# Performance work log

Hardware: AMD Instinct MI355X
Metric: run time of the kernel (lower is better)

The kernel has to match this reference:

```python
import jax, jax.numpy as jnp
import numpy as np

HIDDEN = 512
ATT_DIM = 128
LN_EPS = 1e-3  # keras LayerNormalization default epsilon


def setup_inputs() -> dict:
    key = jax.random.key(0)
    k1, k2, k3, k4 = jax.random.split(key, 4)
    hidden_states = jax.random.normal(k1, (64, 2048, HIDDEN), dtype=jnp.float32)
    # Glorot-uniform style init for the dense weights
    def glorot(k, shape):
        lim = np.sqrt(6.0 / (shape[0] + shape[1]))
        return jax.random.uniform(k, shape, jnp.float32, -lim, lim)
    W_a = glorot(k2, (HIDDEN, ATT_DIM))
    U_a = glorot(k3, (HIDDEN, ATT_DIM))
    v_a = glorot(k4, (ATT_DIM, 1))
    ln_gamma = jnp.ones((HIDDEN,), jnp.float32)
    ln_beta = jnp.zeros((HIDDEN,), jnp.float32)
    return {"hidden_states": hidden_states, "W_a": W_a, "U_a": U_a,
            "v_a": v_a, "ln_gamma": ln_gamma, "ln_beta": ln_beta}


def reference(hidden_states, W_a, U_a, v_a, ln_gamma, ln_beta):
    # hidden_states: (B, L, H)
    h_att = jnp.einsum('blh,ha->bla', hidden_states, W_a)        # (B, L, A)
    context = jnp.mean(hidden_states, axis=1, keepdims=True)     # (B, 1, H)
    u_att = jnp.einsum('blh,ha->bla', context, U_a)              # (B, 1, A) broadcasts
    combined = jnp.tanh(h_att + u_att)                           # (B, L, A)
    scores = jnp.einsum('bla,ao->bl', combined, v_a)             # (B, L)
    attn = jax.nn.softmax(scores, axis=-1)                       # (B, L)
    attended = jnp.einsum('blh,bl->bh', hidden_states, attn)     # (B, H)
    # LayerNormalization over last axis
    mu = jnp.mean(attended, axis=-1, keepdims=True)
    var = jnp.var(attended, axis=-1, keepdims=True)
    normed = (attended - mu) * jax.lax.rsqrt(var + LN_EPS)
    out = normed * ln_gamma + ln_beta
    return out, attn
```

## Files before the change

### kernel.cpp

```cpp
#include <hip/hip_runtime.h>
#include <hip/hip_bf16.h>

#define HIDDEN 512
#define ATT    128
#define NB     64
#define SL     2048
#define LN_EPS 1e-3f

typedef __attribute__((ext_vector_type(8))) short short8;
typedef __attribute__((ext_vector_type(4))) float f32x4;

__device__ __forceinline__ short f2bf(float f) {
    union { float f; unsigned u; } v; v.f = f;
    unsigned r = v.u + 0x7fffu + ((v.u >> 16) & 1u);
    return (short)(r >> 16);
}
__device__ __forceinline__ unsigned pack2bf(float lo, float hi) {
    union { __hip_bfloat162 h; unsigned u; } v;
    v.h = __float22bfloat162_rn(make_float2(lo, hi));
    return v.u;
}
__device__ __forceinline__ float bflo(unsigned u) {
    union { unsigned x; float f; } v; v.x = u << 16; return v.f;
}
__device__ __forceinline__ float bfhi(unsigned u) {
    union { unsigned x; float f; } v; v.x = u & 0xffff0000u; return v.f;
}
__device__ __forceinline__ float tanh_fast(float x) {
    float cx = fminf(fmaxf(x, -15.f), 15.f);
    float e = __expf(2.f * cx);
    return (e - 1.f) * __builtin_amdgcn_rcpf(e + 1.f);
}

__global__ void p0_wt(const float* __restrict__ W, short* __restrict__ Wt) {
    int idx = blockIdx.x * 256 + threadIdx.x;
    int a = idx >> 9, h = idx & 511;
    Wt[idx] = f2bf(W[h * ATT + a]);
}

__launch_bounds__(256, 3)
__global__ void p1_gemm_ctx(const float* __restrict__ hidden, const short* __restrict__ Wt,
                            short* __restrict__ h_att, float* __restrict__ ctx_part) {
    int t = threadIdx.x;
    int wave = t >> 6, lane = t & 63, quad = lane >> 4, cb = lane & 15;
    int row0 = blockIdx.x * 128;

    f32x4 acc[2][8];
    #pragma unroll
    for (int mt = 0; mt < 2; ++mt)
        #pragma unroll
        for (int nt = 0; nt < 8; ++nt)
            acc[mt][nt] = (f32x4){0.f, 0.f, 0.f, 0.f};

    const float* aptr0 = hidden + (size_t)(row0 + wave * 32 + cb) * HIDDEN + quad * 8;
    const float* aptr1 = aptr0 + (size_t)16 * HIDDEN;
    const short* bptr  = Wt + (size_t)cb * HIDDEN + quad * 8;
    float* cptr = ctx_part + (size_t)(blockIdx.x * 4 + wave) * HIDDEN + quad * 8;

    #pragma unroll 2
    for (int k0 = 0; k0 < HIDDEN; k0 += 32) {
        const float4 a0lo = *(const float4*)(aptr0 + k0);
        const float4 a0hi = *(const float4*)(aptr0 + k0 + 4);
        const float4 a1lo = *(const float4*)(aptr1 + k0);
        const float4 a1hi = *(const float4*)(aptr1 + k0 + 4);

        short8 b8[8];
        #pragma unroll
        for (int nt = 0; nt < 8; ++nt)
            b8[nt] = *(const short8*)(bptr + nt * 16 * HIDDEN + k0);

        float s[8] = { a0lo.x + a1lo.x, a0lo.y + a1lo.y, a0lo.z + a1lo.z, a0lo.w + a1lo.w,
                       a0hi.x + a1hi.x, a0hi.y + a1hi.y, a0hi.z + a1hi.z, a0hi.w + a1hi.w };
        #pragma unroll
        for (int j = 0; j < 8; ++j) {
            s[j] += __shfl_xor(s[j], 1);
            s[j] += __shfl_xor(s[j], 2);
            s[j] += __shfl_xor(s[j], 4);
            s[j] += __shfl_xor(s[j], 8);
        }
        if (cb == 0) {
            #pragma unroll
            for (int j = 0; j < 8; ++j) cptr[k0 + j] = s[j];
        }

        union { short8 s8; unsigned u[4]; } a0p, a1p;
        a0p.u[0] = pack2bf(a0lo.x, a0lo.y); a0p.u[1] = pack2bf(a0lo.z, a0lo.w);
        a0p.u[2] = pack2bf(a0hi.x, a0hi.y); a0p.u[3] = pack2bf(a0hi.z, a0hi.w);
        a1p.u[0] = pack2bf(a1lo.x, a1lo.y); a1p.u[1] = pack2bf(a1lo.z, a1lo.w);
        a1p.u[2] = pack2bf(a1hi.x, a1hi.y); a1p.u[3] = pack2bf(a1hi.z, a1hi.w);

        #pragma unroll
        for (int nt = 0; nt < 8; ++nt) {
            acc[0][nt] = __builtin_amdgcn_mfma_f32_16x16x32_bf16(a0p.s8, b8[nt], acc[0][nt], 0, 0, 0);
            acc[1][nt] = __builtin_amdgcn_mfma_f32_16x16x32_bf16(a1p.s8, b8[nt], acc[1][nt], 0, 0, 0);
        }
    }

    uint2* hp = (uint2*)h_att;
    size_t base = (((size_t)blockIdx.x * 4 + wave) * 2) * 8 * 64 + lane;
    #pragma unroll
    for (int mt = 0; mt < 2; ++mt)
        #pragma unroll
        for (int nt = 0; nt < 8; ++nt) {
            uint2 p;
            p.x = pack2bf(acc[mt][nt][0], acc[mt][nt][1]);
            p.y = pack2bf(acc[mt][nt][2], acc[mt][nt][3]);
            hp[base + ((size_t)mt * 8 + nt) * 64] = p;
        }
}

__launch_bounds__(256)
__global__ void p2_uatt(const float* __restrict__ ctx_part, const float* __restrict__ U,
                        float* __restrict__ uatt) {
    int b = blockIdx.x, t = threadIdx.x;
    __shared__ float cs[HIDDEN];
    __shared__ float ds[256];
    float s0 = 0.f, s1 = 0.f;
    #pragma unroll 4
    for (int c = 0; c < 64; ++c) {
        const float* base = ctx_part + (size_t)(b * 64 + c) * HIDDEN;
        s0 += base[t];
        s1 += base[t + 256];
    }
    cs[t] = s0; cs[t + 256] = s1;
    __syncthreads();
    int a = t & 127, h0 = (t >> 7) * 256;
    float d = 0.f;
    #pragma unroll 8
    for (int h = 0; h < 256; ++h) d += cs[h0 + h] * U[(size_t)(h0 + h) * ATT + a];
    ds[t] = d;
    __syncthreads();
    if (t < 128) uatt[b * ATT + t] = (ds[t] + ds[t + 128]) * (1.f / SL);
}

__launch_bounds__(256)
__global__ void p3_scores(const short* __restrict__ h_att, const float* __restrict__ v_a,
                          const float* __restrict__ uatt, float* __restrict__ scores) {
    int t = threadIdx.x, bx = blockIdx.x;
    int wave = t >> 6, lane = t & 63, quad = lane >> 4, cb = lane & 15;
    int b = bx >> 4;
    int row0 = bx * 128;

    float uv[8], vv[8];
    #pragma unroll
    for (int nt = 0; nt < 8; ++nt) {
        uv[nt] = uatt[b * ATT + nt * 16 + cb];
        vv[nt] = v_a[nt * 16 + cb];
    }

    const uint2* hp = (const uint2*)h_att;
    size_t base = (((size_t)bx * 4 + wave) * 2) * 8 * 64 + lane;

    #pragma unroll
    for (int mt = 0; mt < 2; ++mt) {
        uint2 f[8];
        #pragma unroll
        for (int nt = 0; nt < 8; ++nt) f[nt] = hp[base + ((size_t)mt * 8 + nt) * 64];
        float r[4] = {0.f, 0.f, 0.f, 0.f};
        #pragma unroll
        for (int nt = 0; nt < 8; ++nt) {
            r[0] += vv[nt] * tanh_fast(bflo(f[nt].x) + uv[nt]);
            r[1] += vv[nt] * tanh_fast(bfhi(f[nt].x) + uv[nt]);
            r[2] += vv[nt] * tanh_fast(bflo(f[nt].y) + uv[nt]);
            r[3] += vv[nt] * tanh_fast(bfhi(f[nt].y) + uv[nt]);
        }
        #pragma unroll
        for (int j = 0; j < 4; ++j) {
            r[j] += __shfl_xor(r[j], 1);
            r[j] += __shfl_xor(r[j], 2);
            r[j] += __shfl_xor(r[j], 4);
            r[j] += __shfl_xor(r[j], 8);
        }
        if (cb == 0) {
            #pragma unroll
            for (int j = 0; j < 4; ++j)
                scores[row0 + wave * 32 + mt * 16 + quad * 4 + j] = r[j];
        }
    }
}

__launch_bounds__(256)
__global__ void p4_softmax(float* __restrict__ attn) {
    int b = blockIdx.x, t = threadIdx.x;
    float* p = attn + b * SL;
    __shared__ float red[256];
    float v[8];
    float m = -1e30f;
    #pragma unroll
    for (int i = 0; i < 8; ++i) { v[i] = p[t + i * 256]; m = fmaxf(m, v[i]); }
    red[t] = m; __syncthreads();
    for (int s = 128; s > 0; s >>= 1) { if (t < s) red[t] = fmaxf(red[t], red[t + s]); __syncthreads(); }
    m = red[0]; __syncthreads();
    float sum = 0.f;
    #pragma unroll
    for (int i = 0; i < 8; ++i) { v[i] = __expf(v[i] - m); sum += v[i]; }
    red[t] = sum; __syncthreads();
    for (int s = 128; s > 0; s >>= 1) { if (t < s) red[t] += red[t + s]; __syncthreads(); }
    float inv = 1.f / red[0];
    #pragma unroll
    for (int i = 0; i < 8; ++i) p[t + i * 256] = v[i] * inv;
}

__launch_bounds__(256)
__global__ void p5_attended(const float* __restrict__ hidden, const float* __restrict__ attn,
                            float* __restrict__ att_part) {
    int b = blockIdx.y, c = blockIdx.x, t = threadIdx.x;
    __shared__ float w_s[128];
    __shared__ float4 red_s[128];
    if (t < 128) w_s[t] = attn[b * SL + c * 128 + t];
    __syncthreads();
    int cg = t & 127, half = t >> 7;
    const float* hp = hidden + ((size_t)b * SL + c * 128 + half * 64) * HIDDEN + cg * 4;
    float4 a = {0.f, 0.f, 0.f, 0.f};
    #pragma unroll 4
    for (int l = 0; l < 64; ++l) {
        float w = w_s[half * 64 + l];
        const float4 g = *(const float4*)(hp + (size_t)l * HIDDEN);
        a.x += w * g.x; a.y += w * g.y; a.z += w * g.z; a.w += w * g.w;
    }
    if (half) red_s[cg] = a;
    __syncthreads();
    if (!half) {
        float4 r = red_s[cg];
        a.x += r.x; a.y += r.y; a.z += r.z; a.w += r.w;
        *(float4*)(att_part + ((size_t)(c * NB + b)) * HIDDEN + cg * 4) = a;
    }
}

__launch_bounds__(256)
__global__ void p6_ln(const float* __restrict__ att_part, const float* __restrict__ gamma,
                      const float* __restrict__ beta, float* __restrict__ out) {
    int b = blockIdx.x, t = threadIdx.x;
    float x0 = 0.f, x1 = 0.f;
    #pragma unroll
    for (int c = 0; c < 16; ++c) {
        size_t base = (size_t)(c * NB + b) * HIDDEN;
        x0 += att_part[base + t];
        x1 += att_part[base + t + 256];
    }
    __shared__ float rs[256], rq[256];
    rs[t] = x0 + x1; rq[t] = x0 * x0 + x1 * x1;
    __syncthreads();
    for (int s = 128; s > 0; s >>= 1) {
        if (t < s) { rs[t] += rs[t + s]; rq[t] += rq[t + s]; }
        __syncthreads();
    }
    float mean = rs[0] * (1.f / HIDDEN);
    float var = rq[0] * (1.f / HIDDEN) - mean * mean;
    float r = rsqrtf(var + LN_EPS);
    out[b * HIDDEN + t]       = (x0 - mean) * r * gamma[t] + beta[t];
    out[b * HIDDEN + t + 256] = (x1 - mean) * r * gamma[t + 256] + beta[t + 256];
}

extern "C" void kernel_launch(void* const* d_in, const int* in_sizes, int n_in,
                              void* d_out, int out_size, void* d_ws, size_t ws_size,
                              hipStream_t stream) {
    const float* hidden = (const float*)d_in[0];
    const float* W      = (const float*)d_in[1];
    const float* U      = (const float*)d_in[2];
    const float* v_a    = (const float*)d_in[3];
    const float* gamma  = (const float*)d_in[4];
    const float* beta   = (const float*)d_in[5];

    float* out  = (float*)d_out;
    float* attn = out + NB * HIDDEN;

    short* h_att    = (short*)d_ws;
    float* ctx_part = (float*)((char*)d_ws + (size_t)NB * SL * ATT * 2);
    float* att_part = ctx_part + (size_t)4096 * HIDDEN;
    float* uatt     = att_part + (size_t)16 * NB * HIDDEN;
    short* Wt       = (short*)(uatt + NB * ATT);

    p0_wt<<<256, 256, 0, stream>>>(W, Wt);
    p1_gemm_ctx<<<(NB * SL) / 128, 256, 0, stream>>>(hidden, Wt, h_att, ctx_part);
    p2_uatt<<<NB, 256, 0, stream>>>(ctx_part, U, uatt);
    p3_scores<<<(NB * SL) / 128, 256, 0, stream>>>(h_att, v_a, uatt, attn);
    p4_softmax<<<NB, 256, 0, stream>>>(attn);
    p5_attended<<<dim3(16, NB), 256, 0, stream>>>(hidden, attn, att_part);
    p6_ln<<<NB, 256, 0, stream>>>(att_part, gamma, beta, out);
}
```

Before: 504.1 us.

## Stage hidden tiles through swizzled LDS with double buffering and prepacked B fragments

The GEMM+context kernel now loads hidden rows with coalesced row-contiguous float4 loads, converts them to bf16 into a double-buffered, XOR-swizzled shared-memory tile, and prefetches the next 64-column chunk while running MFMAs on the current one. The weight matrix is pre-permuted into MFMA fragment order so each lane reads B with one contiguous 16-byte load. Context partial sums are now reduced across the row subgroup with two shuffles instead of four. This adds 32KB of LDS per block and a barrier per chunk, which may lower occupancy under the launch bounds of 3 blocks.

Result: faster. 478.8 us (-5.0%).

```diff
diff --git a/kernel.cpp b/kernel.cpp
--- a/kernel.cpp
+++ b/kernel.cpp
@@ -32,15 +32,19 @@
     return (e - 1.f) * __builtin_amdgcn_rcpf(e + 1.f);
 }
 
-__global__ void p0_wt(const float* __restrict__ W, short* __restrict__ Wt) {
+__global__ void p0_wt(const float* __restrict__ W, short* __restrict__ Bp) {
     int idx = blockIdx.x * 256 + threadIdx.x;
-    int a = idx >> 9, h = idx & 511;
-    Wt[idx] = f2bf(W[h * ATT + a]);
+    int j = idx & 7, lane = (idx >> 3) & 63, nt = (idx >> 9) & 7, ks = idx >> 12;
+    int a = nt * 16 + (lane & 15);
+    int h = ks * 32 + ((lane >> 4) << 3) + j;
+    Bp[idx] = f2bf(W[h * ATT + a]);
 }
 
 __launch_bounds__(256, 3)
-__global__ void p1_gemm_ctx(const float* __restrict__ hidden, const short* __restrict__ Wt,
+__global__ void p1_gemm_ctx(const float* __restrict__ hidden, const short* __restrict__ Bp,
                             short* __restrict__ h_att, float* __restrict__ ctx_part) {
+    __shared__ __align__(16) short As[2][128 * 64];
+
     int t = threadIdx.x;
     int wave = t >> 6, lane = t & 63, quad = lane >> 4, cb = lane & 15;
     int row0 = blockIdx.x * 128;
@@ -52,48 +56,72 @@
         for (int nt = 0; nt < 8; ++nt)
             acc[mt][nt] = (f32x4){0.f, 0.f, 0.f, 0.f};
 
-    const float* aptr0 = hidden + (size_t)(row0 + wave * 32 + cb) * HIDDEN + quad * 8;
-    const float* aptr1 = aptr0 + (size_t)16 * HIDDEN;
-    const short* bptr  = Wt + (size_t)cb * HIDDEN + quad * 8;
-    float* cptr = ctx_part + (size_t)(blockIdx.x * 4 + wave) * HIDDEN + quad * 8;
-
-    #pragma unroll 2
-    for (int k0 = 0; k0 < HIDDEN; k0 += 32) {
-        const float4 a0lo = *(const float4*)(aptr0 + k0);
-        const float4 a0hi = *(const float4*)(aptr0 + k0 + 4);
-        const float4 a1lo = *(const float4*)(aptr1 + k0);
-        const float4 a1hi = *(const float4*)(aptr1 + k0 + 4);
-
-        short8 b8[8];
-        #pragma unroll
-        for (int nt = 0; nt < 8; ++nt)
-            b8[nt] = *(const short8*)(bptr + nt * 16 * HIDDEN + k0);
-
-        float s[8] = { a0lo.x + a1lo.x, a0lo.y + a1lo.y, a0lo.z + a1lo.z, a0lo.w + a1lo.w,
-                       a0hi.x + a1hi.x, a0hi.y + a1hi.y, a0hi.z + a1hi.z, a0hi.w + a1hi.w };
-        #pragma unroll
-        for (int j = 0; j < 8; ++j) {
-            s[j] += __shfl_xor(s[j], 1);
-            s[j] += __shfl_xor(s[j], 2);
-            s[j] += __shfl_xor(s[j], 4);
-            s[j] += __shfl_xor(s[j], 8);
-        }
-        if (cb == 0) {
+    int rsub = t >> 4;
+    int col4 = t & 15;
+    const float* sbase = hidden + (size_t)(row0 + rsub) * HIDDEN + col4 * 4;
+
+    const short8* Bp8 = (const short8*)Bp + lane;
+
+    float4 g[8];
+
+    auto issue_loads = [&](int c) {
+        const float* src = sbase + c * 64;
+        #pragma unroll
+        for (int p = 0; p < 8; ++p)
+            g[p] = *(const float4*)(src + (size_t)p * 16 * HIDDEN);
+    };
+
+    auto write_and_ctx = [&](int c, int buf) {
+        float s[4] = {0.f, 0.f, 0.f, 0.f};
+        #pragma unroll
+        for (int p = 0; p < 8; ++p) {
+            int row = p * 16 + rsub;
+            const float4 f = g[p];
+            s[0] += f.x; s[1] += f.y; s[2] += f.z; s[3] += f.w;
+            uint2 pk;
+            pk.x = pack2bf(f.x, f.y);
+            pk.y = pack2bf(f.z, f.w);
+            int off = row * 64 + (((col4 >> 1) ^ (row & 7)) << 3) + ((col4 & 1) << 2);
+            *(uint2*)&As[buf][off] = pk;
+        }
+        #pragma unroll
+        for (int j = 0; j < 4; ++j) {
+            s[j] += __shfl_xor(s[j], 16);
+            s[j] += __shfl_xor(s[j], 32);
+        }
+        if (lane < 16) {
+            float* cp = ctx_part + (size_t)(blockIdx.x * 4 + wave) * HIDDEN + c * 64 + lane * 4;
+            *(float4*)cp = (float4){s[0], s[1], s[2], s[3]};
+        }
+    };
+
+    auto compute = [&](int c, int buf) {
+        int ra = wave * 32 + cb;
+        int swz = cb & 7;
+        #pragma unroll
+        for (int s2 = 0; s2 < 2; ++s2) {
+            int blk = ((s2 * 4 + quad) ^ swz) << 3;
+            short8 a0 = *(const short8*)&As[buf][ra * 64 + blk];
+            short8 a1 = *(const short8*)&As[buf][(ra + 16) * 64 + blk];
+            int ks = c * 2 + s2;
             #pragma unroll
-            for (int j = 0; j < 8; ++j) cptr[k0 + j] = s[j];
-        }
-
-        union { short8 s8; unsigned u[4]; } a0p, a1p;
-        a0p.u[0] = pack2bf(a0lo.x, a0lo.y); a0p.u[1] = pack2bf(a0lo.z, a0lo.w);
-        a0p.u[2] = pack2bf(a0hi.x, a0hi.y); a0p.u[3] = pack2bf(a0hi.z, a0hi.w);
-        a1p.u[0] = pack2bf(a1lo.x, a1lo.y); a1p.u[1] = pack2bf(a1lo.z, a1lo.w);
-        a1p.u[2] = pack2bf(a1hi.x, a1hi.y); a1p.u[3] = pack2bf(a1hi.z, a1hi.w);
-
-        #pragma unroll
-        for (int nt = 0; nt < 8; ++nt) {
-            acc[0][nt] = __builtin_amdgcn_mfma_f32_16x16x32_bf16(a0p.s8, b8[nt], acc[0][nt], 0, 0, 0);
-            acc[1][nt] = __builtin_amdgcn_mfma_f32_16x16x32_bf16(a1p.s8, b8[nt], acc[1][nt], 0, 0, 0);
-        }
+            for (int nt = 0; nt < 8; ++nt) {
+                short8 b = Bp8[((size_t)ks * 8 + nt) * 64];
+                acc[0][nt] = __builtin_amdgcn_mfma_f32_16x16x32_bf16(a0, b, acc[0][nt], 0, 0, 0);
+                acc[1][nt] = __builtin_amdgcn_mfma_f32_16x16x32_bf16(a1, b, acc[1][nt], 0, 0, 0);
+            }
+        }
+    };
+
+    issue_loads(0);
+    write_and_ctx(0, 0);
+    __syncthreads();
+
+    for (int c = 0; c < 8; ++c) {
+        if (c < 7) issue_loads(c + 1);
+        compute(c, c & 1);
+        if (c < 7) write_and_ctx(c + 1, (c + 1) & 1);
+        __syncthreads();
     }
 
     uint2* hp = (uint2*)h_att;
@@ -269,10 +297,10 @@
     float* ctx_part = (float*)((char*)d_ws + (size_t)NB * SL * ATT * 2);
     float* att_part = ctx_part + (size_t)4096 * HIDDEN;
     float* uatt     = att_part + (size_t)16 * NB * HIDDEN;
-    short* Wt       = (short*)(uatt + NB * ATT);
-
-    p0_wt<<<256, 256, 0, stream>>>(W, Wt);
-    p1_gemm_ctx<<<(NB * SL) / 128, 256, 0, stream>>>(hidden, Wt, h_att, ctx_part);
+    short* Bp       = (short*)(uatt + NB * ATT);
+
+    p0_wt<<<256, 256, 0, stream>>>(W, Bp);
+    p1_gemm_ctx<<<(NB * SL) / 128, 256, 0, stream>>>(hidden, Bp, h_att, ctx_part);
     p2_uatt<<<NB, 256, 0, stream>>>(ctx_part, U, uatt);
     p3_scores<<<(NB * SL) / 128, 256, 0, stream>>>(h_att, v_a, uatt, attn);
     p4_softmax<<<NB, 256, 0, stream>>>(attn);
```
